# Performance work log

Measured on AMD Instinct MI355X. Metric: run time of the kernel, lower is better.

Reference implementation:

```python
import jax, jax.numpy as jnp
import numpy as np

# Graph / model dims (match init_kwargs config)
N1, N2, N3 = 80000, 16000, 4096
E1, E2 = 256000, 65536
D_IN, H1, C1 = 256, 8, 64   # conv1: concat -> 512
H2, C2 = 4, 64              # conv2: mean over heads -> gnn_outdim=64
F_IN, F_HID, L_DIM, N_CLS = 128, 64, 64, 1


def setup_inputs() -> dict:
    key = jax.random.key(0)
    ks = jax.random.split(key, 20)
    rng = np.random.default_rng(0)

    def edges(E, n_src, n_dst):
        src = rng.integers(0, n_src, size=E)
        dst = rng.integers(0, n_dst, size=E)
        # avoid incidental self loops (PyG remove_self_loops); explicit ones added in conv
        src = np.where(src == dst, src + 1, src)
        return jnp.asarray(src, jnp.int32), jnp.asarray(dst, jnp.int32)

    es1, ed1 = edges(E1, N1, N2)
    es2, ed2 = edges(E2, N2, N3)
    s = 0.05
    return {
        "x": jax.random.normal(ks[0], (N1, D_IN), jnp.float32),
        "flat": jax.random.normal(ks[1], (N3, F_IN), jnp.float32),
        "last": jax.random.normal(ks[2], (N3, L_DIM), jnp.float32),
        "edge_src1": es1, "edge_dst1": ed1,
        "edge_src2": es2, "edge_dst2": ed2,
        "W1_src": jax.random.normal(ks[3], (D_IN, H1 * C1), jnp.float32) * s,
        "W1_dst": jax.random.normal(ks[4], (D_IN, H1 * C1), jnp.float32) * s,
        "att1_src": jax.random.normal(ks[5], (H1, C1), jnp.float32) * s,
        "att1_dst": jax.random.normal(ks[6], (H1, C1), jnp.float32) * s,
        "bias1": jax.random.normal(ks[7], (H1 * C1,), jnp.float32) * s,
        "W2_src": jax.random.normal(ks[8], (H1 * C1, H2 * C2), jnp.float32) * s,
        "W2_dst": jax.random.normal(ks[9], (H1 * C1, H2 * C2), jnp.float32) * s,
        "att2_src": jax.random.normal(ks[10], (H2, C2), jnp.float32) * s,
        "att2_dst": jax.random.normal(ks[11], (H2, C2), jnp.float32) * s,
        "bias2": jax.random.normal(ks[12], (C2,), jnp.float32) * s,
        "flat_W": jax.random.normal(ks[13], (F_IN, F_HID), jnp.float32) * s,
        "flat_b": jax.random.normal(ks[14], (F_HID,), jnp.float32) * s,
        "out_W": jax.random.normal(ks[15], (C2 + F_HID + L_DIM, N_CLS), jnp.float32) * s,
        "out_b": jax.random.normal(ks[16], (N_CLS,), jnp.float32) * s,
    }


def gat_conv(x_src, x_dst, src, dst, W_s, W_d, a_s, a_d, b, concat):
    """PyG bipartite GATConv (eval mode, add_self_loops=True, neg slope 0.2)."""
    H, C = a_s.shape
    Ns, Nd = x_src.shape[0], x_dst.shape[0]
    h_s = (x_src @ W_s).reshape(Ns, H, C)
    h_d = (x_dst @ W_d).reshape(Nd, H, C)
    sl = jnp.arange(Nd, dtype=src.dtype)
    src = jnp.concatenate([src, sl])  # self loops on target nodes
    dst = jnp.concatenate([dst, sl])
    e_s = jnp.einsum("nhc,hc->nh", h_s, a_s)  # [Ns,H]
    e_d = jnp.einsum("nhc,hc->nh", h_d, a_d)  # [Nd,H]
    alpha = jax.nn.leaky_relu(e_s[src] + e_d[dst], negative_slope=0.2)  # [E,H]
    amax = jax.ops.segment_max(alpha, dst, num_segments=Nd)[dst]
    ex = jnp.exp(alpha - amax)
    w = ex / jax.ops.segment_sum(ex, dst, num_segments=Nd)[dst]  # segment softmax
    msg = w[:, :, None] * h_s[src]  # [E,H,C]
    out = jax.ops.segment_sum(msg, dst, num_segments=Nd)  # [Nd,H,C]
    out = out.reshape(Nd, H * C) if concat else out.mean(axis=1)
    return out + b


def reference(x, flat, last, edge_src1, edge_dst1, edge_src2, edge_dst2,
              W1_src, W1_dst, att1_src, att1_dst, bias1,
              W2_src, W2_dst, att2_src, att2_dst, bias2,
              flat_W, flat_b, out_W, out_b):
    # eval mode: featdrop / attndrop / main_dropout are identity
    h = gat_conv(x, x[:N2], edge_src1, edge_dst1,
                 W1_src, W1_dst, att1_src, att1_dst, bias1, concat=True)
    h = jax.nn.elu(h)
    h = gat_conv(h, h[:N3], edge_src2, edge_dst2,
                 W2_src, W2_dst, att2_src, att2_dst, bias2, concat=False)
    f = flat @ flat_W + flat_b
    z = jnp.concatenate([h, f, last], axis=1)  # [N3, 64+64+64]
    return z @ out_W + out_b  # [N3, num_cls]
```

## Files before the change

### kernel.cpp

```cpp
#include <hip/hip_runtime.h>
#include <hip/hip_bf16.h>
#include <cstdio>

typedef __attribute__((ext_vector_type(8))) short short8;
typedef __attribute__((ext_vector_type(4))) short short4v;
typedef __attribute__((ext_vector_type(8))) _Float16 half8;
typedef __attribute__((ext_vector_type(4))) float f32x4;

template <int H> struct VecT;
template <> struct VecT<8> { using T = short8; };
template <> struct VecT<4> { using T = short4v; };

__device__ __forceinline__ float bfu2f(unsigned short u) {
    return __uint_as_float(((unsigned)u) << 16);
}
__device__ __forceinline__ unsigned short f2bfu(float f) {
    __hip_bfloat16 b = __float2bfloat16(f);
    union { __hip_bfloat16 b; unsigned short u; } cv; cv.b = b;
    return cv.u;
}
__device__ __forceinline__ unsigned short f2hu(float f) {
    _Float16 h = (_Float16)f;
    union { _Float16 h; unsigned short u; } cv; cv.h = h;
    return cv.u;
}

#define N1 80000
#define N2 16000
#define N3 4096
#define E1 256000
#define E2 65536

__global__ void prep_kernel(const float* __restrict__ W1s, unsigned short* __restrict__ w1s_pk,
                            const float* __restrict__ W2s, unsigned short* __restrict__ w2s_pk,
                            const float* __restrict__ W1d, const float* __restrict__ a1d,
                            float* __restrict__ v1dT,
                            const float* __restrict__ W2d, const float* __restrict__ a2d,
                            float* __restrict__ v2dT,
                            const float* __restrict__ fW, unsigned short* __restrict__ fw_t3,
                            int* __restrict__ zbase, int zn) {
    int i = blockIdx.x * blockDim.x + threadIdx.x;
    const int S0 = 131072, S1 = 131072, S2 = 8192, S3 = 4096;
    if (i < S0) {
        int k = i >> 9, n = i & 511;
        int n16 = n >> 4, l = n & 15, k32 = k >> 5, qq = (k >> 3) & 3, e = k & 7;
        size_t base = ((size_t)(n16 * 8 + k32)) * 512 + (qq * 16 + l) * 8 + e;
        w1s_pk[base] = f2hu(W1s[i]);
    } else if (i < S0 + S1) {
        int j = i - S0;
        int k = j >> 8, n = j & 255;
        int n16 = n >> 4, l = n & 15, k32 = k >> 5, qq = (k >> 3) & 3, e = k & 7;
        size_t base = ((size_t)(n16 * 16 + k32)) * 512 + (qq * 16 + l) * 8 + e;
        w2s_pk[base] = f2hu(W2s[j]);
    } else if (i < S0 + S1 + S2) {
        int j = i - S0 - S1;
        int k = j >> 6, n = j & 63;
        float v = fW[j];
        unsigned short h = f2bfu(v);
        unsigned short l = f2bfu(v - bfu2f(h));
        size_t base = (size_t)n * 384;
        fw_t3[base + k] = h;
        fw_t3[base + 128 + k] = l;
        fw_t3[base + 256 + k] = h;
    } else if (i < S0 + S1 + S2 + S3) {
        int j = i - S0 - S1 - S2;
        if (j < 2048) {
            int h = j >> 8, k = j & 255;
            float s = 0.f;
            for (int c = 0; c < 64; c++) s += W1d[k * 512 + h * 64 + c] * a1d[h * 64 + c];
            v1dT[j] = s;
        } else {
            int jj = j - 2048;
            int h = jj >> 9, k = jj & 511;
            float s = 0.f;
            for (int c = 0; c < 64; c++) s += W2d[k * 256 + h * 64 + c] * a2d[h * 64 + c];
            v2dT[jj] = s;
        }
    } else {
        int j = i - S0 - S1 - S2 - S3;
        if (j < zn) zbase[j] = 0;
    }
}

__global__ void hist_dual(const int* __restrict__ d1, int* __restrict__ c1,
                          const int* __restrict__ d2, int* __restrict__ c2) {
    int i = blockIdx.x * blockDim.x + threadIdx.x;
    if (i < E1) {
        int d = d1[i];
        if ((unsigned)d < (unsigned)N2) atomicAdd(&c1[d], 1);
    } else if (i < E1 + E2) {
        int d = d2[i - E1];
        if ((unsigned)d < (unsigned)N3) atomicAdd(&c2[d], 1);
    }
}
__global__ __launch_bounds__(1024)
void scan_dual(const int* __restrict__ c1, int* __restrict__ s1, int Nd1,
               const int* __restrict__ c2, int* __restrict__ s2, int Nd2) {
    const int* cnt = (blockIdx.x == 0) ? c1 : c2;
    int* start = (blockIdx.x == 0) ? s1 : s2;
    int Nd = (blockIdx.x == 0) ? Nd1 : Nd2;
    __shared__ int part[1024];
    int t = threadIdx.x;
    int k = (Nd + 1023) >> 10;
    int lo = t * k, hi = min(lo + k, Nd);
    if (lo > Nd) lo = Nd;
    int s = 0;
    for (int i = lo; i < hi; i++) s += cnt[i];
    part[t] = s;
    __syncthreads();
    for (int off = 1; off < 1024; off <<= 1) {
        int v = (t >= off) ? part[t - off] : 0;
        __syncthreads();
        part[t] += v;
        __syncthreads();
    }
    int run = (t > 0) ? part[t - 1] : 0;
    for (int i = lo; i < hi; i++) { start[i] = run; run += cnt[i]; }
    if (t == 1023) start[Nd] = part[1023];
}
__global__ void fill_dual(const int* __restrict__ sa1, const int* __restrict__ da1,
                          const int* __restrict__ st1, int* __restrict__ cu1, int* __restrict__ cs1,
                          const int* __restrict__ sa2, const int* __restrict__ da2,
                          const int* __restrict__ st2, int* __restrict__ cu2, int* __restrict__ cs2) {
    int i = blockIdx.x * blockDim.x + threadIdx.x;
    const int *sa, *da, *st;
    int *cu, *cs;
    int Nd, Ns, e;
    if (i < E1) { sa = sa1; da = da1; st = st1; cu = cu1; cs = cs1; Nd = N2; Ns = N1; e = i; }
    else if (i < E1 + E2) { sa = sa2; da = da2; st = st2; cu = cu2; cs = cs2; Nd = N3; Ns = N2; e = i - E1; }
    else return;
    int d = da[e];
    if ((unsigned)d >= (unsigned)Nd) return;
    int p = atomicAdd(&cu[d], 1);
    int idx = st[d] + p;
    if (idx >= st[d + 1]) return;
    int s = sa[e];
    if ((unsigned)s >= (unsigned)Ns) s = 0;
    cs[idx] = s;
}

template <bool AF16>
__device__ __forceinline__ void gemm_core(_Float16 (*As)[64][72],
              const void* __restrict__ Ax,
              const unsigned short* __restrict__ Bp, unsigned short* __restrict__ C,
              const float* __restrict__ att, float* __restrict__ es_out,
              int MT, int NB, int N, int K, int H, int hb) {
    const int xcd = hb & 7;
    const int sI = hb >> 3;
    const int mt = (sI / NB) * 8 + xcd;
    const int nb = sI % NB;
    if (mt >= MT) return;
    const int m0 = mt * 64;
    const int tid = threadIdx.x;
    const int wave = tid >> 6, lane = tid & 63;
    const int q = lane >> 4, l15 = lane & 15;
    const int n0 = nb * 256 + wave * 64;
    const int KS = K >> 6;
    const int KSB = K >> 5;
    const int arow = tid >> 2, ac16 = (tid & 3) * 16;
    const unsigned short* Bbase = Bp + (size_t)(n0 >> 4) * KSB * 512 + lane * 8;

    f32x4 acc[4][4] = {};
    half8 b[2][4];
    float4 s0, s1, s2, s3;
    half8 sh0, sh1;

    auto stageLoad = [&](int t) {
        if constexpr (AF16) {
            const _Float16* p = (const _Float16*)Ax + (size_t)(m0 + arow) * K + t * 64 + ac16;
            sh0 = *(const half8*)p;
            sh1 = *(const half8*)(p + 8);
        } else {
            const float* p = (const float*)Ax + (size_t)(m0 + arow) * K + t * 64 + ac16;
            s0 = *(const float4*)p;
            s1 = *(const float4*)(p + 4);
            s2 = *(const float4*)(p + 8);
            s3 = *(const float4*)(p + 12);
        }
    };
    auto stageWrite = [&](int buf) {
        half8 v0, v1;
        if constexpr (AF16) {
            v0 = sh0; v1 = sh1;
        } else {
            v0[0] = (_Float16)s0.x; v0[1] = (_Float16)s0.y;
            v0[2] = (_Float16)s0.z; v0[3] = (_Float16)s0.w;
            v0[4] = (_Float16)s1.x; v0[5] = (_Float16)s1.y;
            v0[6] = (_Float16)s1.z; v0[7] = (_Float16)s1.w;
            v1[0] = (_Float16)s2.x; v1[1] = (_Float16)s2.y;
            v1[2] = (_Float16)s2.z; v1[3] = (_Float16)s2.w;
            v1[4] = (_Float16)s3.x; v1[5] = (_Float16)s3.y;
            v1[6] = (_Float16)s3.z; v1[7] = (_Float16)s3.w;
        }
        *(half8*)&As[buf][arow][ac16] = v0;
        *(half8*)&As[buf][arow][ac16 + 8] = v1;
    };
    auto loadB = [&](int k32, int kh, int nt) {
        b[kh][nt] = *(const half8*)(Bbase + ((size_t)nt * KSB + k32) * 512);
    };

    stageLoad(0);
#pragma unroll
    for (int kh = 0; kh < 2; kh++)
#pragma unroll
        for (int nt = 0; nt < 4; nt++) loadB(kh, kh, nt);
    stageWrite(0);
    __syncthreads();

    int cur = 0;
    for (int t = 0; t < KS; t++) {
        const bool hn = (t + 1) < KS;
        if (hn) stageLoad(t + 1);
#pragma unroll
        for (int kh = 0; kh < 2; kh++) {
#pragma unroll
            for (int rg = 0; rg < 4; rg++) {
                half8 a = *(const half8*)&As[cur][rg * 16 + l15][kh * 32 + q * 8];
#pragma unroll
                for (int nt = 0; nt < 4; nt++) {
                    acc[rg][nt] = __builtin_amdgcn_mfma_f32_16x16x32_f16(a, b[kh][nt], acc[rg][nt], 0, 0, 0);
                    if (rg == 3 && hn) loadB(2 * (t + 1) + kh, kh, nt);
                }
            }
        }
        if (hn) {
            stageWrite(cur ^ 1);
            __syncthreads();
        }
        cur ^= 1;
    }

#pragma unroll
    for (int rg = 0; rg < 4; rg++)
#pragma unroll
        for (int nt = 0; nt < 4; nt++)
#pragma unroll
            for (int r = 0; r < 4; r++) {
                int row = m0 + rg * 16 + q * 4 + r;
                int col = n0 + nt * 16 + l15;
                C[(size_t)row * N + col] = f2bfu(acc[rg][nt][r]);
            }
    {
        const int head = n0 >> 6;
        float av[4];
#pragma unroll
        for (int nt = 0; nt < 4; nt++) av[nt] = att[head * 64 + nt * 16 + l15];
#pragma unroll
        for (int rg = 0; rg < 4; rg++)
#pragma unroll
            for (int r = 0; r < 4; r++) {
                float p = acc[rg][0][r] * av[0] + acc[rg][1][r] * av[1]
                        + acc[rg][2][r] * av[2] + acc[rg][3][r] * av[3];
#pragma unroll
                for (int off = 1; off < 16; off <<= 1) p += __shfl_xor(p, off);
                if (l15 == 0)
                    es_out[(size_t)(m0 + rg * 16 + q * 4 + r) * H + head] = p;
            }
    }
}

__global__ __launch_bounds__(256, 2)
void gemm_l1(const void* __restrict__ Ax,
             const unsigned short* __restrict__ Bp, unsigned short* __restrict__ C,
             const float* __restrict__ att, float* __restrict__ es_out,
             int MT, int NB, int N, int K, int H) {
    __shared__ alignas(16) _Float16 As[2][64][72];
    gemm_core<false>(As, Ax, Bp, C, att, es_out, MT, NB, N, K, H, blockIdx.x);
}

__device__ __forceinline__ void flat_core(unsigned char* smemraw,
        const float* __restrict__ A, const unsigned short* __restrict__ Bt3,
        float* __restrict__ C, int mb) {
    const int K = 128, N = 64, KK = 384;
    auto As = (unsigned short (*)[64][72])smemraw;
    auto Bs = (unsigned short (*)[72])(smemraw + 18432);
    const int tid = threadIdx.x;
    const int wave = tid >> 6, lane = tid & 63;
    const int wr = wave >> 1, wc = wave & 1;
    const int quad = lane >> 4, l15 = lane & 15;
    const int m0 = mb * 64, n0 = 0;
    f32x4 acc[2][2] = {};
    for (int k0 = 0; k0 < KK; k0 += 64) {
        const int seg = k0 / K;
        const int ks = k0 - seg * K;
#pragma unroll
        for (int i = 0; i < 2; i++) {
            int idx = tid + i * 256;
            int r = idx >> 3, cv = (idx & 7) * 8;
            const float* ap = &A[(size_t)(m0 + r) * K + ks + cv];
            const float4 v0 = *(const float4*)ap;
            const float4 v1 = *(const float4*)(ap + 4);
            float va[8] = {v0.x, v0.y, v0.z, v0.w, v1.x, v1.y, v1.z, v1.w};
            short8 h8, l8;
#pragma unroll
            for (int j = 0; j < 8; j++) {
                unsigned short hh = f2bfu(va[j]);
                h8[j] = (short)hh;
                l8[j] = (short)f2bfu(va[j] - bfu2f(hh));
            }
            *(short8*)&As[0][r][cv] = h8;
            *(short8*)&As[1][r][cv] = l8;
            *(short8*)&Bs[r][cv] = *(const short8*)&Bt3[(size_t)(n0 + r) * KK + k0 + cv];
        }
        __syncthreads();
        const int abank = (seg < 2) ? 0 : 1;
#pragma unroll
        for (int kk = 0; kk < 64; kk += 32) {
            short8 a[2], b[2];
#pragma unroll
            for (int t = 0; t < 2; t++) {
                a[t] = *(const short8*)&As[abank][wr * 32 + t * 16 + l15][kk + quad * 8];
                b[t] = *(const short8*)&Bs[wc * 32 + t * 16 + l15][kk + quad * 8];
            }
#pragma unroll
            for (int mt = 0; mt < 2; mt++)
#pragma unroll
                for (int nt = 0; nt < 2; nt++)
                    acc[mt][nt] = __builtin_amdgcn_mfma_f32_16x16x32_bf16(
                        a[mt], b[nt], acc[mt][nt], 0, 0, 0);
        }
        __syncthreads();
    }
#pragma unroll
    for (int mt = 0; mt < 2; mt++)
#pragma unroll
        for (int nt = 0; nt < 2; nt++)
#pragma unroll
            for (int r = 0; r < 4; r++) {
                int row = m0 + wr * 32 + mt * 16 + quad * 4 + r;
                int col = n0 + wc * 32 + nt * 16 + l15;
                C[(size_t)row * N + col] = acc[mt][nt][r];
            }
}

__global__ __launch_bounds__(256, 2)
void gemm2_flat(const void* __restrict__ Ax,
                const unsigned short* __restrict__ Bp, unsigned short* __restrict__ C,
                const float* __restrict__ att, float* __restrict__ es_out,
                int MT, int NB, int N, int K, int H, int G2,
                const float* __restrict__ fA, const unsigned short* __restrict__ fBt3,
                float* __restrict__ fC) {
    __shared__ alignas(16) unsigned char smem[27648];
    if ((int)blockIdx.x < G2) {
        gemm_core<true>((_Float16(*)[64][72])smem, Ax, Bp, C, att, es_out,
                        MT, NB, N, K, H, blockIdx.x);
    } else {
        flat_core(smem, fA, fBt3, fC, blockIdx.x - G2);
    }
}

template <int H, bool ELU, bool HOUT, bool XF16, int KD, bool FIN>
__global__ __launch_bounds__(256)
void gat_agg2(const int* __restrict__ csr, const int* __restrict__ rs,
              const unsigned short* __restrict__ hs,
              const float* __restrict__ es,
              const void* __restrict__ xsrc,
              const float* __restrict__ vdT,
              const float* __restrict__ bias,
              void* __restrict__ out,
              int Nd,
              const float* __restrict__ fbuf, const float* __restrict__ flat_b,
              const float* __restrict__ last, const float* __restrict__ outW,
              const float* __restrict__ outb, float* __restrict__ fout) {
    constexpr int LH = (H == 8) ? 3 : 2;
    constexpr int EPC = 64 >> LH;
    constexpr int KPL = KD / EPC;
    const int lane = threadIdx.x & 63;
    const int d = blockIdx.x * (blockDim.x >> 6) + (threadIdx.x >> 6);
    if (d >= Nd) return;
    const int h = lane & (H - 1);
    const int e0 = lane >> LH;
    float edh = 0.f;
    {
        const float* vp = vdT + h * KD + e0 * KPL;
        if constexpr (XF16) {
            const _Float16* xr = (const _Float16*)xsrc + (size_t)d * KD + e0 * KPL;
#pragma unroll
            for (int i8 = 0; i8 < KPL / 8; i8++) {
                half8 hx = *(const half8*)(xr + i8 * 8);
#pragma unroll
                for (int jj = 0; jj < 8; jj++) edh += (float)hx[jj] * vp[i8 * 8 + jj];
            }
        } else {
            const float* xr = (const float*)xsrc + (size_t)d * KD + e0 * KPL;
#pragma unroll
            for (int i4 = 0; i4 < KPL / 4; i4++) {
                float4 xv = *(const float4*)(xr + i4 * 4);
                float4 vv = *(const float4*)(vp + i4 * 4);
                edh += xv.x * vv.x + xv.y * vv.y + xv.z * vv.z + xv.w * vv.w;
            }
        }
#pragma unroll
        for (int off = H; off < 64; off <<= 1) edh += __shfl_xor(edh, off);
    }
    const int beg = rs[d];
    const int deg = rs[d + 1] - beg;
    const int n = deg + 1;
    const int nch = (n + EPC - 1) / EPC;
    const int hB = lane >> (6 - LH);
    using V = typename VecT<H>::T;
    float acc[H] = {};
    const size_t rowoff = (size_t)lane * H;
    if (nch <= 8) {
        float ac[8];
        float mx = -1e30f;
#pragma unroll
        for (int c = 0; c < 8; c++) {
            float a = -1e30f;
            if (c < nch) {
                int j = c * EPC + e0;
                if (j < n) {
                    int s = (j < deg) ? csr[beg + j] : d;
                    a = es[(size_t)s * H + h] + edh;
                    a = (a > 0.0f) ? a : 0.2f * a;
                }
            }
            ac[c] = a;
            mx = fmaxf(mx, a);
        }
#pragma unroll
        for (int off = H; off < 64; off <<= 1) mx = fmaxf(mx, __shfl_xor(mx, off));
        float den = 0.0f;
#pragma unroll
        for (int c = 0; c < 8; c++)
            if (c < nch) den += expf(ac[c] - mx);
#pragma unroll
        for (int off = H; off < 64; off <<= 1) den += __shfl_xor(den, off);
        const float inv = 1.0f / den;
        float ec[8];
#pragma unroll
        for (int c = 0; c < 8; c++) ec[c] = expf(ac[c] - mx) * inv;
#pragma unroll
        for (int c = 0; c < 8; c++) {
            if (c >= nch) break;
            const int jb = c * EPC;
            int s[EPC]; V rv[EPC];
#pragma unroll
            for (int u = 0; u < EPC; u++) {
                int jj = jb + u;
                s[u] = (jj < deg) ? csr[beg + jj] : d;
            }
#pragma unroll
            for (int u = 0; u < EPC; u++)
                rv[u] = *(const V*)&hs[(size_t)s[u] * (H * 64) + rowoff];
#pragma unroll
            for (int u = 0; u < EPC; u++) {
                float w = __shfl(ec[c], u * H + hB);
#pragma unroll
                for (int k = 0; k < H; k++) acc[k] += w * bfu2f((unsigned short)rv[u][k]);
            }
        }
    } else {
        float mx = -1e30f;
        for (int j0 = 0; j0 < n; j0 += EPC) {
            int j = j0 + e0;
            if (j < n) {
                int s = (j < deg) ? csr[beg + j] : d;
                float a = es[(size_t)s * H + h] + edh;
                a = (a > 0.0f) ? a : 0.2f * a;
                mx = fmaxf(mx, a);
            }
        }
#pragma unroll
        for (int off = H; off < 64; off <<= 1) mx = fmaxf(mx, __shfl_xor(mx, off));
        float den = 0.0f;
        for (int j0 = 0; j0 < n; j0 += EPC) {
            int j = j0 + e0;
            if (j < n) {
                int s = (j < deg) ? csr[beg + j] : d;
                float a = es[(size_t)s * H + h] + edh;
                a = (a > 0.0f) ? a : 0.2f * a;
                den += expf(a - mx);
            }
        }
#pragma unroll
        for (int off = H; off < 64; off <<= 1) den += __shfl_xor(den, off);
        const float inv = 1.0f / den;
        const float mB = __shfl(mx, hB);
        const float invB = __shfl(inv, hB);
        const float edhB = __shfl(edh, hB);
        int j = 0;
        for (; j + 4 <= n; j += 4) {
            int s[4]; V rv[4]; float w[4];
#pragma unroll
            for (int u = 0; u < 4; u++) { int jj = j + u; s[u] = (jj < deg) ? csr[beg + jj] : d; }
#pragma unroll
            for (int u = 0; u < 4; u++) rv[u] = *(const V*)&hs[(size_t)s[u] * (H * 64) + rowoff];
#pragma unroll
            for (int u = 0; u < 4; u++) {
                float a = es[(size_t)s[u] * H + hB] + edhB;
                a = (a > 0.0f) ? a : 0.2f * a;
                w[u] = expf(a - mB) * invB;
            }
#pragma unroll
            for (int u = 0; u < 4; u++)
#pragma unroll
                for (int k = 0; k < H; k++) acc[k] += w[u] * bfu2f((unsigned short)rv[u][k]);
        }
        for (; j < n; j++) {
            int s = (j < deg) ? csr[beg + j] : d;
            V rv = *(const V*)&hs[(size_t)s * (H * 64) + rowoff];
            float a = es[(size_t)s * H + hB] + edhB;
            a = (a > 0.0f) ? a : 0.2f * a;
            float w = expf(a - mB) * invB;
#pragma unroll
            for (int k = 0; k < H; k++) acc[k] += w * bfu2f((unsigned short)rv[k]);
        }
    }
    if constexpr (FIN) {
        float f4[4];
#pragma unroll
        for (int k = 0; k < 4; k++) {
            float a2v = acc[k] + __shfl_xor(acc[k], 32);
            f4[k] = a2v + __shfl_xor(a2v, 16);
        }
        float part = 0.f;
        if (lane < 16) {
            const int c0 = lane * 4;
            float4 fb4 = *(const float4*)&fbuf[(size_t)d * 64 + c0];
            float4 lb4 = *(const float4*)&last[(size_t)d * 64 + c0];
            const float* fbv = &fb4.x;
            const float* lbv = &lb4.x;
#pragma unroll
            for (int k = 0; k < 4; k++) {
                int c = c0 + k;
                float h2 = 0.25f * f4[k] + bias[c];
                part += h2 * outW[c];
                part += (fbv[k] + flat_b[c]) * outW[64 + c];
                part += lbv[k] * outW[128 + c];
            }
        }
#pragma unroll
        for (int off = 1; off < 16; off <<= 1) part += __shfl_xor(part, off);
        if (lane == 0) fout[d] = part + outb[0];
    } else {
#pragma unroll
        for (int k = 0; k < H; k++) {
            float v = acc[k];
            if (ELU) {
                v += bias[lane * H + k];
                v = (v > 0.0f) ? v : expm1f(v);
            }
            acc[k] = v;
        }
        if constexpr (HOUT) {
            half8 hv;
#pragma unroll
            for (int k = 0; k < H; k++) hv[k] = (_Float16)acc[k];
            _Float16* op = (_Float16*)out + (size_t)d * (H * 64) + rowoff;
            *(half8*)op = hv;
        } else {
            float* op = (float*)out + (size_t)d * (H * 64) + rowoff;
#pragma unroll
            for (int qd = 0; qd < H / 4; qd++)
                *(float4*)&op[qd * 4] = *(float4*)&acc[qd * 4];
        }
    }
}

extern "C" void kernel_launch(void* const* d_in, const int* in_sizes, int n_in,
                              void* d_out, int out_size, void* d_ws, size_t ws_size,
                              hipStream_t stream) {
    const float* x    = (const float*)d_in[0];
    const float* flat = (const float*)d_in[1];
    const float* last = (const float*)d_in[2];
    const int*  es1i  = (const int*)d_in[3];
    const int*  ed1i  = (const int*)d_in[4];
    const int*  es2i  = (const int*)d_in[5];
    const int*  ed2i  = (const int*)d_in[6];
    const float* W1s  = (const float*)d_in[7];
    const float* W1d  = (const float*)d_in[8];
    const float* a1s  = (const float*)d_in[9];
    const float* a1d  = (const float*)d_in[10];
    const float* b1   = (const float*)d_in[11];
    const float* W2s  = (const float*)d_in[12];
    const float* W2d  = (const float*)d_in[13];
    const float* a2s  = (const float*)d_in[14];
    const float* a2d  = (const float*)d_in[15];
    const float* b2   = (const float*)d_in[16];
    const float* fW   = (const float*)d_in[17];
    const float* fb   = (const float*)d_in[18];
    const float* oW   = (const float*)d_in[19];
    const float* ob   = (const float*)d_in[20];
    float* out = (float*)d_out;

    float* ws = (float*)d_ws;
    unsigned short* hs1_bf = (unsigned short*)ws;
    float* es1f = ws + 24576000;
    float* acc1 = ws + 25344000;
    unsigned short* wb = (unsigned short*)(ws + 54016000);
    unsigned short* w1s_pk = wb;
    unsigned short* w2s_pk = wb + 524288;
    unsigned short* fw_t3  = wb + 1048576;
    float* v1dT = ws + 54600000;
    float* v2dT = ws + 54602048;
    int* ibase   = (int*)(ws + 54816000);
    int* cnt1    = ibase;
    int* cursor1 = ibase + 16000;
    int* cnt2    = ibase + 32000;
    int* cursor2 = ibase + 36096;
    int* start1  = ibase + 40192;
    int* start2  = ibase + 56193;
    int* csr1    = ibase + 60290;
    int* csr2    = ibase + 316290;
    const size_t NEED = ((size_t)54816000 + 381826) * 4;
    if (ws_size < NEED) {
        fprintf(stderr, "kernel_launch: ws_size %zu < needed %zu\n", ws_size, NEED);
        return;
    }
    unsigned short* hs2_bf = (unsigned short*)ws;
    float* es2f = ws + 2572288;
    float* fbuf = ws + 3701248;
    unsigned short* acc1h = (unsigned short*)acc1;

    {
        int total = 131072 + 131072 + 8192 + 4096 + 40192;
        prep_kernel<<<(total + 255) / 256, 256, 0, stream>>>(
            W1s, w1s_pk, W2s, w2s_pk,
            W1d, a1d, v1dT, W2d, a2d, v2dT,
            fW, fw_t3, ibase, 40192);
    }
    hist_dual<<<(E1 + E2 + 255) / 256, 256, 0, stream>>>(ed1i, cnt1, ed2i, cnt2);
    scan_dual<<<2, 1024, 0, stream>>>(cnt1, start1, N2, cnt2, start2, N3);
    fill_dual<<<(E1 + E2 + 255) / 256, 256, 0, stream>>>(
        es1i, ed1i, start1, cursor1, csr1, es2i, ed2i, start2, cursor2, csr2);

    {
        const int MT = N1 / 64;
        const int NB = 2;
        const int grid = 8 * NB * ((MT + 7) / 8);
        gemm_l1<<<grid, 256, 0, stream>>>(
            x, w1s_pk, hs1_bf, a1s, es1f, MT, NB, 512, 256, 8);
    }
    gat_agg2<8, true, true, false, 256, false><<<N2 / 4, 256, 0, stream>>>(
        csr1, start1, hs1_bf, es1f, x, v1dT, b1, acc1h, N2,
        nullptr, nullptr, nullptr, nullptr, nullptr, nullptr);

    {
        const int MT = N2 / 64;
        const int G2 = 8 * ((MT + 7) / 8);
        gemm2_flat<<<G2 + N3 / 64, 256, 0, stream>>>(
            acc1h, w2s_pk, hs2_bf, a2s, es2f, MT, 1, 256, 512, 4, G2,
            flat, fw_t3, fbuf);
    }
    gat_agg2<4, false, false, true, 512, true><<<N3 / 4, 256, 0, stream>>>(
        csr2, start2, hs2_bf, es2f, acc1h, v2dT, b2, nullptr, N3,
        fbuf, fb, last, oW, ob, out);
}
```

Measured before the change: 350.7 us.

## Fuse prep/hist, fill and dst-score into GEMM launches; fp16 features with dot2 aggregation

Merges the prep and histogram kernels into one launch and folds CSR fill plus per-destination attention scores into the layer GEMM launches as extra blocks. This removes separate launches and takes the dst-score dot products out of the aggregation kernels. Zeroing moves to hipMemsetAsync. Intermediate features are now stored as fp16 instead of bf16, so aggregation can use packed fdot2 with double-buffered chunk loads, which trades some accumulation precision for fewer instructions.

```diff
diff --git a/kernel.cpp b/kernel.cpp
--- a/kernel.cpp
+++ b/kernel.cpp
@@ -3,13 +3,17 @@
 #include <cstdio>
 
 typedef __attribute__((ext_vector_type(8))) short short8;
-typedef __attribute__((ext_vector_type(4))) short short4v;
 typedef __attribute__((ext_vector_type(8))) _Float16 half8;
+typedef __attribute__((ext_vector_type(2))) __fp16 fp16x2;
 typedef __attribute__((ext_vector_type(4))) float f32x4;
-
-template <int H> struct VecT;
-template <> struct VecT<8> { using T = short8; };
-template <> struct VecT<4> { using T = short4v; };
+typedef __attribute__((ext_vector_type(4))) unsigned int uint4v;
+typedef __attribute__((ext_vector_type(2))) unsigned int uint2v;
+
+#if defined(__has_builtin)
+#if __has_builtin(__builtin_amdgcn_fdot2) && __has_builtin(__builtin_amdgcn_perm) && __has_builtin(__builtin_amdgcn_cvt_pkrtz)
+#define USE_DOT2 1
+#endif
+#endif
 
 __device__ __forceinline__ float bfu2f(unsigned short u) {
     return __uint_as_float(((unsigned)u) << 16);
@@ -24,6 +28,21 @@
     union { _Float16 h; unsigned short u; } cv; cv.h = h;
     return cv.u;
 }
+__device__ __forceinline__ float hu2f(unsigned short u) {
+    union { unsigned short u; _Float16 h; } cv; cv.u = u;
+    return (float)cv.h;
+}
+#ifdef USE_DOT2
+__device__ __forceinline__ unsigned pkw(float w0, float w1) {
+    union { fp16x2 v; unsigned u; } cv;
+    cv.v = __builtin_amdgcn_cvt_pkrtz(w0, w1);
+    return cv.u;
+}
+__device__ __forceinline__ float fdot2acc(unsigned a, unsigned b, float c) {
+    union { unsigned u; fp16x2 v; } ua, ub; ua.u = a; ub.u = b;
+    return __builtin_amdgcn_fdot2(ua.v, ub.v, c, false);
+}
+#endif
 
 #define N1 80000
 #define N2 16000
@@ -31,68 +50,68 @@
 #define E1 256000
 #define E2 65536
 
-__global__ void prep_kernel(const float* __restrict__ W1s, unsigned short* __restrict__ w1s_pk,
-                            const float* __restrict__ W2s, unsigned short* __restrict__ w2s_pk,
-                            const float* __restrict__ W1d, const float* __restrict__ a1d,
-                            float* __restrict__ v1dT,
-                            const float* __restrict__ W2d, const float* __restrict__ a2d,
-                            float* __restrict__ v2dT,
-                            const float* __restrict__ fW, unsigned short* __restrict__ fw_t3,
-                            int* __restrict__ zbase, int zn) {
-    int i = blockIdx.x * blockDim.x + threadIdx.x;
-    const int S0 = 131072, S1 = 131072, S2 = 8192, S3 = 4096;
-    if (i < S0) {
-        int k = i >> 9, n = i & 511;
-        int n16 = n >> 4, l = n & 15, k32 = k >> 5, qq = (k >> 3) & 3, e = k & 7;
-        size_t base = ((size_t)(n16 * 8 + k32)) * 512 + (qq * 16 + l) * 8 + e;
-        w1s_pk[base] = f2hu(W1s[i]);
-    } else if (i < S0 + S1) {
-        int j = i - S0;
-        int k = j >> 8, n = j & 255;
-        int n16 = n >> 4, l = n & 15, k32 = k >> 5, qq = (k >> 3) & 3, e = k & 7;
-        size_t base = ((size_t)(n16 * 16 + k32)) * 512 + (qq * 16 + l) * 8 + e;
-        w2s_pk[base] = f2hu(W2s[j]);
-    } else if (i < S0 + S1 + S2) {
-        int j = i - S0 - S1;
-        int k = j >> 6, n = j & 63;
-        float v = fW[j];
-        unsigned short h = f2bfu(v);
-        unsigned short l = f2bfu(v - bfu2f(h));
-        size_t base = (size_t)n * 384;
-        fw_t3[base + k] = h;
-        fw_t3[base + 128 + k] = l;
-        fw_t3[base + 256 + k] = h;
-    } else if (i < S0 + S1 + S2 + S3) {
-        int j = i - S0 - S1 - S2;
-        if (j < 2048) {
-            int h = j >> 8, k = j & 255;
-            float s = 0.f;
-            for (int c = 0; c < 64; c++) s += W1d[k * 512 + h * 64 + c] * a1d[h * 64 + c];
-            v1dT[j] = s;
+__global__ void prep_hist(const float* __restrict__ W1s, unsigned short* __restrict__ w1s_pk,
+                          const float* __restrict__ W2s, unsigned short* __restrict__ w2s_pk,
+                          const float* __restrict__ W1d, const float* __restrict__ a1d,
+                          float* __restrict__ v1dT,
+                          const float* __restrict__ W2d, const float* __restrict__ a2d,
+                          float* __restrict__ v2dT,
+                          const float* __restrict__ fW, unsigned short* __restrict__ fw_t3,
+                          int PB,
+                          const int* __restrict__ ed1i, int* __restrict__ cnt1,
+                          const int* __restrict__ ed2i, int* __restrict__ cnt2) {
+    const int bid = blockIdx.x;
+    if (bid < PB) {
+        int i = bid * 256 + threadIdx.x;
+        const int S0 = 131072, S1 = 131072, S2 = 8192;
+        if (i < S0) {
+            int k = i >> 9, n = i & 511;
+            int n16 = n >> 4, l = n & 15, k32 = k >> 5, qq = (k >> 3) & 3, e = k & 7;
+            size_t base = ((size_t)(n16 * 8 + k32)) * 512 + (qq * 16 + l) * 8 + e;
+            w1s_pk[base] = f2hu(W1s[i]);
+        } else if (i < S0 + S1) {
+            int j = i - S0;
+            int k = j >> 8, n = j & 255;
+            int n16 = n >> 4, l = n & 15, k32 = k >> 5, qq = (k >> 3) & 3, e = k & 7;
+            size_t base = ((size_t)(n16 * 16 + k32)) * 512 + (qq * 16 + l) * 8 + e;
+            w2s_pk[base] = f2hu(W2s[j]);
+        } else if (i < S0 + S1 + S2) {
+            int j = i - S0 - S1;
+            int k = j >> 6, n = j & 63;
+            float v = fW[j];
+            unsigned short h = f2bfu(v);
+            unsigned short l = f2bfu(v - bfu2f(h));
+            size_t base = (size_t)n * 384;
+            fw_t3[base + k] = h;
+            fw_t3[base + 128 + k] = l;
+            fw_t3[base + 256 + k] = h;
         } else {
-            int jj = j - 2048;
-            int h = jj >> 9, k = jj & 511;
-            float s = 0.f;
-            for (int c = 0; c < 64; c++) s += W2d[k * 256 + h * 64 + c] * a2d[h * 64 + c];
-            v2dT[jj] = s;
+            int j = i - S0 - S1 - S2;
+            if (j < 2048) {
+                int h = j >> 8, k = j & 255;
+                float s = 0.f;
+                for (int c = 0; c < 64; c++) s += W1d[k * 512 + h * 64 + c] * a1d[h * 64 + c];
+                v1dT[j] = s;
+            } else if (j < 4096) {
+                int jj = j - 2048;
+                int h = jj >> 9, k = jj & 511;
+                float s = 0.f;
+                for (int c = 0; c < 64; c++) s += W2d[k * 256 + h * 64 + c] * a2d[h * 64 + c];
+                v2dT[jj] = s;
+            }
         }
     } else {
-        int j = i - S0 - S1 - S2 - S3;
-        if (j < zn) zbase[j] = 0;
-    }
-}
-
-__global__ void hist_dual(const int* __restrict__ d1, int* __restrict__ c1,
-                          const int* __restrict__ d2, int* __restrict__ c2) {
-    int i = blockIdx.x * blockDim.x + threadIdx.x;
-    if (i < E1) {
-        int d = d1[i];
-        if ((unsigned)d < (unsigned)N2) atomicAdd(&c1[d], 1);
-    } else if (i < E1 + E2) {
-        int d = d2[i - E1];
-        if ((unsigned)d < (unsigned)N3) atomicAdd(&c2[d], 1);
-    }
-}
+        int i = (bid - PB) * 256 + threadIdx.x;
+        if (i < E1) {
+            int d = ed1i[i];
+            if ((unsigned)d < (unsigned)N2) atomicAdd(&cnt1[d], 1);
+        } else if (i < E1 + E2) {
+            int d = ed2i[i - E1];
+            if ((unsigned)d < (unsigned)N3) atomicAdd(&cnt2[d], 1);
+        }
+    }
+}
+
 __global__ __launch_bounds__(1024)
 void scan_dual(const int* __restrict__ c1, int* __restrict__ s1, int Nd1,
                const int* __restrict__ c2, int* __restrict__ s2, int Nd2) {
@@ -118,11 +137,13 @@
     for (int i = lo; i < hi; i++) { start[i] = run; run += cnt[i]; }
     if (t == 1023) start[Nd] = part[1023];
 }
-__global__ void fill_dual(const int* __restrict__ sa1, const int* __restrict__ da1,
-                          const int* __restrict__ st1, int* __restrict__ cu1, int* __restrict__ cs1,
-                          const int* __restrict__ sa2, const int* __restrict__ da2,
-                          const int* __restrict__ st2, int* __restrict__ cu2, int* __restrict__ cs2) {
-    int i = blockIdx.x * blockDim.x + threadIdx.x;
+
+__device__ __forceinline__ void fill_core(int fb,
+        const int* __restrict__ sa1, const int* __restrict__ da1,
+        const int* __restrict__ st1, int* __restrict__ cu1, int* __restrict__ cs1,
+        const int* __restrict__ sa2, const int* __restrict__ da2,
+        const int* __restrict__ st2, int* __restrict__ cu2, int* __restrict__ cs2) {
+    int i = fb * 256 + threadIdx.x;
     const int *sa, *da, *st;
     int *cu, *cs;
     int Nd, Ns, e;
@@ -137,6 +158,72 @@
     int s = sa[e];
     if ((unsigned)s >= (unsigned)Ns) s = 0;
     cs[idx] = s;
+}
+
+__device__ __forceinline__ void ed1_core(const float* __restrict__ x, const float* __restrict__ v1dT,
+                                         float* __restrict__ ed1, int blk) {
+    const int lane = threadIdx.x & 63;
+    const int w = threadIdx.x >> 6;
+    float4 vv[8];
+#pragma unroll
+    for (int h = 0; h < 8; h++) vv[h] = *(const float4*)&v1dT[h * 256 + lane * 4];
+    for (int i = 0; i < 4; i++) {
+        int d = blk * 16 + w * 4 + i;
+        if (d >= N2) return;
+        float4 xv = *(const float4*)&x[(size_t)d * 256 + lane * 4];
+        float p[8];
+#pragma unroll
+        for (int h = 0; h < 8; h++)
+            p[h] = xv.x * vv[h].x + xv.y * vv[h].y + xv.z * vv[h].z + xv.w * vv[h].w;
+#pragma unroll
+        for (int off = 1; off < 64; off <<= 1)
+#pragma unroll
+            for (int h = 0; h < 8; h++) p[h] += __shfl_xor(p[h], off);
+        if (lane < 8) {
+            int hh = lane;
+            float a01 = (hh & 1) ? p[1] : p[0], a23 = (hh & 1) ? p[3] : p[2];
+            float a45 = (hh & 1) ? p[5] : p[4], a67 = (hh & 1) ? p[7] : p[6];
+            float b0 = (hh & 2) ? a23 : a01, b1 = (hh & 2) ? a67 : a45;
+            ed1[d * 8 + hh] = (hh & 4) ? b1 : b0;
+        }
+    }
+}
+__device__ __forceinline__ void ed2_core(const unsigned short* __restrict__ xh,
+                                         const float* __restrict__ v2dT,
+                                         float* __restrict__ ed2, int blk) {
+    const int lane = threadIdx.x & 63;
+    const int w = threadIdx.x >> 6;
+    float vv[4][8];
+#pragma unroll
+    for (int h = 0; h < 4; h++)
+#pragma unroll
+        for (int j = 0; j < 8; j++) vv[h][j] = v2dT[h * 512 + lane * 8 + j];
+    for (int i = 0; i < 4; i++) {
+        int d = blk * 16 + w * 4 + i;
+        if (d >= N3) return;
+        uint4v rw = *(const uint4v*)&xh[(size_t)d * 512 + lane * 8];
+        const unsigned short* rb = (const unsigned short*)&rw;
+        float xf[8];
+#pragma unroll
+        for (int j = 0; j < 8; j++) xf[j] = hu2f(rb[j]);
+        float p[4];
+#pragma unroll
+        for (int h = 0; h < 4; h++) {
+            float s = 0.f;
+#pragma unroll
+            for (int j = 0; j < 8; j++) s += xf[j] * vv[h][j];
+            p[h] = s;
+        }
+#pragma unroll
+        for (int off = 1; off < 64; off <<= 1)
+#pragma unroll
+            for (int h = 0; h < 4; h++) p[h] += __shfl_xor(p[h], off);
+        if (lane < 4) {
+            int hh = lane;
+            float a01 = (hh & 1) ? p[1] : p[0], a23 = (hh & 1) ? p[3] : p[2];
+            ed2[d * 4 + hh] = (hh & 2) ? a23 : a01;
+        }
+    }
 }
 
 template <bool AF16>
@@ -238,7 +325,7 @@
             for (int r = 0; r < 4; r++) {
                 int row = m0 + rg * 16 + q * 4 + r;
                 int col = n0 + nt * 16 + l15;
-                C[(size_t)row * N + col] = f2bfu(acc[rg][nt][r]);
+                C[(size_t)row * N + col] = f2hu(acc[rg][nt][r]);
             }
     {
         const int head = n0 >> 6;
@@ -260,12 +347,19 @@
 }
 
 __global__ __launch_bounds__(256, 2)
-void gemm_l1(const void* __restrict__ Ax,
-             const unsigned short* __restrict__ Bp, unsigned short* __restrict__ C,
-             const float* __restrict__ att, float* __restrict__ es_out,
-             int MT, int NB, int N, int K, int H) {
+void gemm1_fused(const void* __restrict__ Ax,
+                 const unsigned short* __restrict__ Bp, unsigned short* __restrict__ C,
+                 const float* __restrict__ att, float* __restrict__ es_out,
+                 int MT, int NB, int N, int K, int H, int G1, int FB,
+                 const int* sa1, const int* da1, const int* st1, int* cu1, int* cs1,
+                 const int* sa2, const int* da2, const int* st2, int* cu2, int* cs2,
+                 const float* __restrict__ xe, const float* __restrict__ v1dT,
+                 float* __restrict__ ed1) {
     __shared__ alignas(16) _Float16 As[2][64][72];
-    gemm_core<false>(As, Ax, Bp, C, att, es_out, MT, NB, N, K, H, blockIdx.x);
+    const int bid = blockIdx.x;
+    if (bid < G1) gemm_core<false>(As, Ax, Bp, C, att, es_out, MT, NB, N, K, H, bid);
+    else if (bid < G1 + FB) fill_core(bid - G1, sa1, da1, st1, cu1, cs1, sa2, da2, st2, cu2, cs2);
+    else ed1_core(xe, v1dT, ed1, bid - G1 - FB);
 }
 
 __device__ __forceinline__ void flat_core(unsigned char* smemraw,
@@ -334,121 +428,130 @@
 }
 
 __global__ __launch_bounds__(256, 2)
-void gemm2_flat(const void* __restrict__ Ax,
-                const unsigned short* __restrict__ Bp, unsigned short* __restrict__ C,
-                const float* __restrict__ att, float* __restrict__ es_out,
-                int MT, int NB, int N, int K, int H, int G2,
-                const float* __restrict__ fA, const unsigned short* __restrict__ fBt3,
-                float* __restrict__ fC) {
+void gemm2_fused(const void* __restrict__ Ax,
+                 const unsigned short* __restrict__ Bp, unsigned short* __restrict__ C,
+                 const float* __restrict__ att, float* __restrict__ es_out,
+                 int MT, int NB, int N, int K, int H, int G2, int FLB,
+                 const float* __restrict__ fA, const unsigned short* __restrict__ fBt3,
+                 float* __restrict__ fC,
+                 const unsigned short* __restrict__ x2h, const float* __restrict__ v2dT,
+                 float* __restrict__ ed2) {
     __shared__ alignas(16) unsigned char smem[27648];
-    if ((int)blockIdx.x < G2) {
-        gemm_core<true>((_Float16(*)[64][72])smem, Ax, Bp, C, att, es_out,
-                        MT, NB, N, K, H, blockIdx.x);
-    } else {
-        flat_core(smem, fA, fBt3, fC, blockIdx.x - G2);
-    }
-}
-
-template <int H, bool ELU, bool HOUT, bool XF16, int KD, bool FIN>
+    const int bid = blockIdx.x;
+    if (bid < G2) gemm_core<true>((_Float16(*)[64][72])smem, Ax, Bp, C, att, es_out,
+                                  MT, NB, N, K, H, bid);
+    else if (bid < G2 + FLB) flat_core(smem, fA, fBt3, fC, bid - G2);
+    else ed2_core(x2h, v2dT, ed2, bid - G2 - FLB);
+}
+
+template <int H, bool ELU, bool HOUT, bool FIN>
 __global__ __launch_bounds__(256)
-void gat_agg2(const int* __restrict__ csr, const int* __restrict__ rs,
+void gat_agg3(const int* __restrict__ csr, const int* __restrict__ rs,
               const unsigned short* __restrict__ hs,
               const float* __restrict__ es,
-              const void* __restrict__ xsrc,
-              const float* __restrict__ vdT,
+              const float* __restrict__ edv,
               const float* __restrict__ bias,
-              void* __restrict__ out,
-              int Nd,
+              void* __restrict__ out, int Nd,
               const float* __restrict__ fbuf, const float* __restrict__ flat_b,
               const float* __restrict__ last, const float* __restrict__ outW,
               const float* __restrict__ outb, float* __restrict__ fout) {
     constexpr int LH = (H == 8) ? 3 : 2;
     constexpr int EPC = 64 >> LH;
-    constexpr int KPL = KD / EPC;
+    constexpr int ND = H / 2;
     const int lane = threadIdx.x & 63;
-    const int d = blockIdx.x * (blockDim.x >> 6) + (threadIdx.x >> 6);
+    const int d = blockIdx.x * 4 + (threadIdx.x >> 6);
     if (d >= Nd) return;
     const int h = lane & (H - 1);
     const int e0 = lane >> LH;
-    float edh = 0.f;
-    {
-        const float* vp = vdT + h * KD + e0 * KPL;
-        if constexpr (XF16) {
-            const _Float16* xr = (const _Float16*)xsrc + (size_t)d * KD + e0 * KPL;
-#pragma unroll
-            for (int i8 = 0; i8 < KPL / 8; i8++) {
-                half8 hx = *(const half8*)(xr + i8 * 8);
-#pragma unroll
-                for (int jj = 0; jj < 8; jj++) edh += (float)hx[jj] * vp[i8 * 8 + jj];
-            }
-        } else {
-            const float* xr = (const float*)xsrc + (size_t)d * KD + e0 * KPL;
-#pragma unroll
-            for (int i4 = 0; i4 < KPL / 4; i4++) {
-                float4 xv = *(const float4*)(xr + i4 * 4);
-                float4 vv = *(const float4*)(vp + i4 * 4);
-                edh += xv.x * vv.x + xv.y * vv.y + xv.z * vv.z + xv.w * vv.w;
-            }
-        }
-#pragma unroll
-        for (int off = H; off < 64; off <<= 1) edh += __shfl_xor(edh, off);
-    }
+    const int hB = lane >> (6 - LH);
+    const float edh = edv[(size_t)d * H + h];
     const int beg = rs[d];
     const int deg = rs[d + 1] - beg;
     const int n = deg + 1;
     const int nch = (n + EPC - 1) / EPC;
-    const int hB = lane >> (6 - LH);
-    using V = typename VecT<H>::T;
     float acc[H] = {};
     const size_t rowoff = (size_t)lane * H;
     if (nch <= 8) {
-        float ac[8];
-        float mx = -1e30f;
+        int idxA = d, idxB = d;
+        if (lane < deg) idxA = csr[beg + lane];
+        if constexpr (H == 4) { if (64 + lane < deg) idxB = csr[beg + 64 + lane]; }
+        float av[8];
 #pragma unroll
         for (int c = 0; c < 8; c++) {
+            if (c < nch) {
+                int jv = c * EPC + e0;
+                int s;
+                if (c * EPC + EPC - 1 < 64) s = __shfl(idxA, jv);
+                else s = __shfl(idxB, jv - 64);
+                av[c] = es[(size_t)s * H + h];
+            }
+        }
+        unsigned rvA[EPC][ND], rvB[EPC][ND];
+        auto loadChunk = [&](int c, unsigned (&rv)[EPC][ND]) {
+#pragma unroll
+            for (int u = 0; u < EPC; u++) {
+                int src = c * EPC + u;
+                int s = (src < 64) ? __shfl(idxA, src) : __shfl(idxB, src - 64);
+                const unsigned short* rp = &hs[(size_t)s * (H * 64) + rowoff];
+                if constexpr (H == 8) *(uint4v*)&rv[u][0] = *(const uint4v*)rp;
+                else *(uint2v*)&rv[u][0] = *(const uint2v*)rp;
+            }
+        };
+        loadChunk(0, rvA);
+        float al[8], mx = -1e30f;
+#pragma unroll
+        for (int c = 0; c < 8; c++) {
+            int jv = c * EPC + e0;
             float a = -1e30f;
-            if (c < nch) {
-                int j = c * EPC + e0;
-                if (j < n) {
-                    int s = (j < deg) ? csr[beg + j] : d;
-                    a = es[(size_t)s * H + h] + edh;
-                    a = (a > 0.0f) ? a : 0.2f * a;
+            if (c < nch && jv < n) { a = av[c] + edh; a = (a > 0.f) ? a : 0.2f * a; }
+            al[c] = a;
+            mx = fmaxf(mx, a);
+        }
+#pragma unroll
+        for (int off = H; off < 64; off <<= 1) mx = fmaxf(mx, __shfl_xor(mx, off));
+        float exv[8], den = 0.f;
+#pragma unroll
+        for (int c = 0; c < 8; c++) { exv[c] = expf(al[c] - mx); den += exv[c]; }
+#pragma unroll
+        for (int off = H; off < 64; off <<= 1) den += __shfl_xor(den, off);
+        const float inv = 1.f / den;
+        float ec[8];
+#pragma unroll
+        for (int c = 0; c < 8; c++) ec[c] = exv[c] * inv;
+        auto computeChunk = [&](int c, unsigned (&rv)[EPC][ND]) {
+#pragma unroll
+            for (int pu = 0; pu < EPC / 2; pu++) {
+                float w0 = __shfl(ec[c], (2 * pu) * H + hB);
+                float w1 = __shfl(ec[c], (2 * pu + 1) * H + hB);
+#ifdef USE_DOT2
+                unsigned w2 = pkw(w0, w1);
+#pragma unroll
+                for (int dwi = 0; dwi < ND; dwi++) {
+                    unsigned lo = __builtin_amdgcn_perm(rv[2 * pu + 1][dwi], rv[2 * pu][dwi], 0x05040100u);
+                    unsigned hi = __builtin_amdgcn_perm(rv[2 * pu + 1][dwi], rv[2 * pu][dwi], 0x07060302u);
+                    acc[2 * dwi] = fdot2acc(w2, lo, acc[2 * dwi]);
+                    acc[2 * dwi + 1] = fdot2acc(w2, hi, acc[2 * dwi + 1]);
                 }
-            }
-            ac[c] = a;
-            mx = fmaxf(mx, a);
-        }
-#pragma unroll
-        for (int off = H; off < 64; off <<= 1) mx = fmaxf(mx, __shfl_xor(mx, off));
-        float den = 0.0f;
-#pragma unroll
-        for (int c = 0; c < 8; c++)
-            if (c < nch) den += expf(ac[c] - mx);
-#pragma unroll
-        for (int off = H; off < 64; off <<= 1) den += __shfl_xor(den, off);
-        const float inv = 1.0f / den;
-        float ec[8];
-#pragma unroll
-        for (int c = 0; c < 8; c++) ec[c] = expf(ac[c] - mx) * inv;
-#pragma unroll
-        for (int c = 0; c < 8; c++) {
+#else
+#pragma unroll
+                for (int dwi = 0; dwi < ND; dwi++) {
+                    unsigned q0 = rv[2 * pu][dwi], q1 = rv[2 * pu + 1][dwi];
+                    acc[2 * dwi]     += w0 * hu2f((unsigned short)(q0 & 0xffff))
+                                      + w1 * hu2f((unsigned short)(q1 & 0xffff));
+                    acc[2 * dwi + 1] += w0 * hu2f((unsigned short)(q0 >> 16))
+                                      + w1 * hu2f((unsigned short)(q1 >> 16));
+                }
+#endif
+            }
+        };
+#pragma unroll
+        for (int c = 0; c < 8; c += 2) {
             if (c >= nch) break;
-            const int jb = c * EPC;
-            int s[EPC]; V rv[EPC];
-#pragma unroll
-            for (int u = 0; u < EPC; u++) {
-                int jj = jb + u;
-                s[u] = (jj < deg) ? csr[beg + jj] : d;
-            }
-#pragma unroll
-            for (int u = 0; u < EPC; u++)
-                rv[u] = *(const V*)&hs[(size_t)s[u] * (H * 64) + rowoff];
-#pragma unroll
-            for (int u = 0; u < EPC; u++) {
-                float w = __shfl(ec[c], u * H + hB);
-#pragma unroll
-                for (int k = 0; k < H; k++) acc[k] += w * bfu2f((unsigned short)rv[u][k]);
-            }
+            if (c + 1 < nch) loadChunk(c + 1, rvB);
+            computeChunk(c, rvA);
+            if (c + 1 >= nch) break;
+            if (c + 2 < nch) loadChunk(c + 2, rvA);
+            computeChunk(c + 1, rvB);
         }
     } else {
         float mx = -1e30f;
@@ -479,32 +582,14 @@
         const float mB = __shfl(mx, hB);
         const float invB = __shfl(inv, hB);
         const float edhB = __shfl(edh, hB);
-        int j = 0;
-        for (; j + 4 <= n; j += 4) {
-            int s[4]; V rv[4]; float w[4];
-#pragma unroll
-            for (int u = 0; u < 4; u++) { int jj = j + u; s[u] = (jj < deg) ? csr[beg + jj] : d; }
-#pragma unroll
-            for (int u = 0; u < 4; u++) rv[u] = *(const V*)&hs[(size_t)s[u] * (H * 64) + rowoff];
-#pragma unroll
-            for (int u = 0; u < 4; u++) {
-                float a = es[(size_t)s[u] * H + hB] + edhB;
-                a = (a > 0.0f) ? a : 0.2f * a;
-                w[u] = expf(a - mB) * invB;
-            }
-#pragma unroll
-            for (int u = 0; u < 4; u++)
-#pragma unroll
-                for (int k = 0; k < H; k++) acc[k] += w[u] * bfu2f((unsigned short)rv[u][k]);
-        }
-        for (; j < n; j++) {
+        for (int j = 0; j < n; j++) {
             int s = (j < deg) ? csr[beg + j] : d;
-            V rv = *(const V*)&hs[(size_t)s * (H * 64) + rowoff];
+            const unsigned short* rp = &hs[(size_t)s * (H * 64) + rowoff];
             float a = es[(size_t)s * H + hB] + edhB;
             a = (a > 0.0f) ? a : 0.2f * a;
             float w = expf(a - mB) * invB;
 #pragma unroll
-            for (int k = 0; k < H; k++) acc[k] += w * bfu2f((unsigned short)rv[k]);
+            for (int k = 0; k < H; k++) acc[k] += w * hu2f(rp[k]);
         }
     }
     if constexpr (FIN) {
@@ -585,8 +670,9 @@
     float* out = (float*)d_out;
 
     float* ws = (float*)d_ws;
-    unsigned short* hs1_bf = (unsigned short*)ws;
+    unsigned short* hs1_h = (unsigned short*)ws;
     float* es1f = ws + 24576000;
+    float* ed1f = ws + 25216000;
     float* acc1 = ws + 25344000;
     unsigned short* wb = (unsigned short*)(ws + 54016000);
     unsigned short* w1s_pk = wb;
@@ -608,42 +694,49 @@
         fprintf(stderr, "kernel_launch: ws_size %zu < needed %zu\n", ws_size, NEED);
         return;
     }
-    unsigned short* hs2_bf = (unsigned short*)ws;
+    unsigned short* hs2_h = (unsigned short*)ws;
     float* es2f = ws + 2572288;
+    float* ed2f = ws + 2636288;
     float* fbuf = ws + 3701248;
     unsigned short* acc1h = (unsigned short*)acc1;
 
+    (void)hipMemsetAsync(ibase, 0, 40192 * sizeof(int), stream);
     {
-        int total = 131072 + 131072 + 8192 + 4096 + 40192;
-        prep_kernel<<<(total + 255) / 256, 256, 0, stream>>>(
+        const int PB = 1072;
+        const int HB = (E1 + E2) / 256;
+        prep_hist<<<PB + HB, 256, 0, stream>>>(
             W1s, w1s_pk, W2s, w2s_pk,
             W1d, a1d, v1dT, W2d, a2d, v2dT,
-            fW, fw_t3, ibase, 40192);
-    }
-    hist_dual<<<(E1 + E2 + 255) / 256, 256, 0, stream>>>(ed1i, cnt1, ed2i, cnt2);
+            fW, fw_t3, PB, ed1i, cnt1, ed2i, cnt2);
+    }
     scan_dual<<<2, 1024, 0, stream>>>(cnt1, start1, N2, cnt2, start2, N3);
-    fill_dual<<<(E1 + E2 + 255) / 256, 256, 0, stream>>>(
-        es1i, ed1i, start1, cursor1, csr1, es2i, ed2i, start2, cursor2, csr2);
 
     {
         const int MT = N1 / 64;
         const int NB = 2;
-        const int grid = 8 * NB * ((MT + 7) / 8);
-        gemm_l1<<<grid, 256, 0, stream>>>(
-            x, w1s_pk, hs1_bf, a1s, es1f, MT, NB, 512, 256, 8);
-    }
-    gat_agg2<8, true, true, false, 256, false><<<N2 / 4, 256, 0, stream>>>(
-        csr1, start1, hs1_bf, es1f, x, v1dT, b1, acc1h, N2,
+        const int G1 = 8 * NB * ((MT + 7) / 8);
+        const int FB = (E1 + E2) / 256;
+        const int EB = N2 / 16;
+        gemm1_fused<<<G1 + FB + EB, 256, 0, stream>>>(
+            x, w1s_pk, hs1_h, a1s, es1f, MT, NB, 512, 256, 8, G1, FB,
+            es1i, ed1i, start1, cursor1, csr1, es2i, ed2i, start2, cursor2, csr2,
+            x, v1dT, ed1f);
+    }
+    gat_agg3<8, true, true, false><<<N2 / 4, 256, 0, stream>>>(
+        csr1, start1, hs1_h, es1f, ed1f, b1, acc1h, N2,
         nullptr, nullptr, nullptr, nullptr, nullptr, nullptr);
 
     {
         const int MT = N2 / 64;
         const int G2 = 8 * ((MT + 7) / 8);
-        gemm2_flat<<<G2 + N3 / 64, 256, 0, stream>>>(
-            acc1h, w2s_pk, hs2_bf, a2s, es2f, MT, 1, 256, 512, 4, G2,
-            flat, fw_t3, fbuf);
-    }
-    gat_agg2<4, false, false, true, 512, true><<<N3 / 4, 256, 0, stream>>>(
-        csr2, start2, hs2_bf, es2f, acc1h, v2dT, b2, nullptr, N3,
+        const int FLB = N3 / 64;
+        const int EB2 = N3 / 16;
+        gemm2_fused<<<G2 + FLB + EB2, 256, 0, stream>>>(
+            acc1h, w2s_pk, hs2_h, a2s, es2f, MT, 1, 256, 512, 4, G2, FLB,
+            flat, fw_t3, fbuf,
+            acc1h, v2dT, ed2f);
+    }
+    gat_agg3<4, false, false, true><<<N3 / 4, 256, 0, stream>>>(
+        csr2, start2, hs2_h, es2f, ed2f, b2, nullptr, N3,
         fbuf, fb, last, oW, ob, out);
 }
```

Measured after the change: 322.4 us. 8.1% less time.
